# Kernel optimization log

Hardware: AMD Instinct MI355X
Metric: run time of the kernel (lower is better)

## Reference

```python
import jax, jax.numpy as jnp
import numpy as np

N = 100000   # nodes
E = 1000000  # edges per block
P = 100000   # pos/neg link edges
IN = 128
H = 64


def setup_inputs() -> dict:
    key = jax.random.key(0)
    ks = jax.random.split(key, 24)
    d = {}
    d["x"] = jax.random.normal(ks[0], (N, IN), jnp.float32)
    d["edge_weight"] = jax.random.uniform(ks[1], (3, E), jnp.float32)
    d["src"] = jax.random.randint(ks[2], (E,), 0, N)
    d["dst"] = jax.random.randint(ks[3], (E,), 0, N)
    d["pos_src"] = jax.random.randint(ks[4], (P,), 0, N)
    d["pos_dst"] = jax.random.randint(ks[5], (P,), 0, N)
    d["neg_src"] = jax.random.randint(ks[6], (P,), 0, N)
    d["neg_dst"] = jax.random.randint(ks[7], (P,), 0, N)
    s = 1.0 / np.sqrt(IN)
    h = 1.0 / np.sqrt(H)
    d["W0"] = jax.random.normal(ks[8], (IN, H), jnp.float32) * s
    d["b0"] = jnp.zeros((H,), jnp.float32)
    d["W1"] = jax.random.normal(ks[9], (H, H), jnp.float32) * h
    d["b1"] = jnp.zeros((H,), jnp.float32)
    d["W2"] = jax.random.normal(ks[10], (H, H), jnp.float32) * h
    d["b2"] = jnp.zeros((H,), jnp.float32)
    d["P0"] = jax.random.normal(ks[11], (H, H), jnp.float32) * h
    d["pb0"] = jnp.zeros((H,), jnp.float32)
    d["P1"] = jax.random.normal(ks[12], (H, H), jnp.float32) * h
    d["pb1"] = jnp.zeros((H,), jnp.float32)
    d["P2"] = jax.random.normal(ks[13], (H, 1), jnp.float32) * h
    d["pb2"] = jnp.zeros((1,), jnp.float32)
    return d


def _graph_conv(h, W, b, src, dst, ew, n_nodes):
    # DGL GraphConv, norm='both': D_out^{-1/2} on source feats,
    # edge-weighted sum aggregation, D_in^{-1/2} on result, then linear.
    ones = jnp.ones(src.shape[0], h.dtype)
    deg_out = jax.ops.segment_sum(ones, src, num_segments=n_nodes)
    deg_in = jax.ops.segment_sum(ones, dst, num_segments=n_nodes)
    norm_src = jax.lax.rsqrt(jnp.maximum(deg_out, 1.0))
    norm_dst = jax.lax.rsqrt(jnp.maximum(deg_in, 1.0))
    # apply weight before aggregation (in_feats >= out_feats); math-equivalent either way
    hw = (h * norm_src[:, None]) @ W            # [N, H]
    msg = hw[src] * ew[:, None]                 # [E, H] gather + scale
    agg = jax.ops.segment_sum(msg, dst, num_segments=n_nodes)  # scatter-add
    return agg * norm_dst[:, None] + b


def reference(x, edge_weight, src, dst, pos_src, pos_dst, neg_src, neg_dst,
              W0, b0, W1, b1, W2, b2, P0, pb0, P1, pb1, P2, pb2):
    h = jax.nn.relu(_graph_conv(x, W0, b0, src, dst, edge_weight[0], N))
    h = jax.nn.relu(_graph_conv(h, W1, b1, src, dst, edge_weight[1], N))
    h = _graph_conv(h, W2, b2, src, dst, edge_weight[2], N)  # no relu on last layer

    def mlp(z):
        z = jax.nn.relu(z @ P0 + pb0)
        z = jax.nn.relu(z @ P1 + pb1)
        return z @ P2 + pb2

    h_pos = mlp(h[pos_src] * h[pos_dst])  # [P, 1]
    h_neg = mlp(h[neg_src] * h[neg_dst])  # [P, 1]
    return (h_pos, h_neg)
```

## Files before the change

### kernel.cpp

```cpp
#include <hip/hip_runtime.h>


#define NN 100000
#define NE 1000000
#define NP 100000
#define SCAN_NB 98

__device__ __forceinline__ void row_fma(float4& acc, float xv, const float4& wv) {
    acc.x = fmaf(xv, wv.x, acc.x);
    acc.y = fmaf(xv, wv.y, acc.y);
    acc.z = fmaf(xv, wv.z, acc.z);
    acc.w = fmaf(xv, wv.w, acc.w);
}

__global__ void deg_kernel(const int4* __restrict__ src4, const int4* __restrict__ dst4,
                           int* __restrict__ repl, int E4) {
    int xcc;
    asm volatile("s_getreg_b32 %0, hwreg(HW_REG_XCC_ID)" : "=s"(xcc));
    xcc &= 7;
    int* dout = repl + xcc * NN;
    int* din  = repl + (8 + xcc) * NN;
    int tid = blockIdx.x * blockDim.x + threadIdx.x;
    if (tid < E4) {
        int4 s = src4[tid], d = dst4[tid];
        __hip_atomic_fetch_add(&dout[s.x], 1, __ATOMIC_RELAXED, __HIP_MEMORY_SCOPE_WORKGROUP);
        __hip_atomic_fetch_add(&dout[s.y], 1, __ATOMIC_RELAXED, __HIP_MEMORY_SCOPE_WORKGROUP);
        __hip_atomic_fetch_add(&dout[s.z], 1, __ATOMIC_RELAXED, __HIP_MEMORY_SCOPE_WORKGROUP);
        __hip_atomic_fetch_add(&dout[s.w], 1, __ATOMIC_RELAXED, __HIP_MEMORY_SCOPE_WORKGROUP);
        __hip_atomic_fetch_add(&din[d.x], 1, __ATOMIC_RELAXED, __HIP_MEMORY_SCOPE_WORKGROUP);
        __hip_atomic_fetch_add(&din[d.y], 1, __ATOMIC_RELAXED, __HIP_MEMORY_SCOPE_WORKGROUP);
        __hip_atomic_fetch_add(&din[d.z], 1, __ATOMIC_RELAXED, __HIP_MEMORY_SCOPE_WORKGROUP);
        __hip_atomic_fetch_add(&din[d.w], 1, __ATOMIC_RELAXED, __HIP_MEMORY_SCOPE_WORKGROUP);
    }
}

__global__ void reduce_norm_kernel(const int* __restrict__ repl, float* __restrict__ norm_src,
                                   float* __restrict__ norm_dst, int* __restrict__ deg_in, int n) {
    int i = blockIdx.x * blockDim.x + threadIdx.x;
    if (i < n) {
        int so = 0, si = 0;
#pragma unroll
        for (int x = 0; x < 8; ++x) {
            so += repl[x * NN + i];
            si += repl[(8 + x) * NN + i];
        }
        norm_src[i] = rsqrtf(fmaxf((float)so, 1.0f));
        norm_dst[i] = rsqrtf(fmaxf((float)si, 1.0f));
        deg_in[i] = si;
    }
}

__global__ __launch_bounds__(1024) void scan_block(const int* __restrict__ deg,
                                                   int* __restrict__ tmp_excl,
                                                   int* __restrict__ blocksums, int n) {
    __shared__ int wsums[16];
    const int i = blockIdx.x * 1024 + threadIdx.x;
    const int lane = threadIdx.x & 63, w = threadIdx.x >> 6;
    int v = (i < n) ? deg[i] : 0;
    int s = v;
#pragma unroll
    for (int off = 1; off < 64; off <<= 1) {
        int u = __shfl_up(s, off, 64);
        if (lane >= off) s += u;
    }
    if (lane == 63) wsums[w] = s;
    __syncthreads();
    if (w == 0) {
        int wv = (lane < 16) ? wsums[lane] : 0;
#pragma unroll
        for (int off = 1; off < 16; off <<= 1) {
            int u = __shfl_up(wv, off, 64);
            if (lane >= off) wv += u;
        }
        if (lane < 16) wsums[lane] = wv;
    }
    __syncthreads();
    int excl = s - v + (w > 0 ? wsums[w - 1] : 0);
    if (i < n) tmp_excl[i] = excl;
    if (threadIdx.x == 1023) blocksums[blockIdx.x] = excl + v;
}

__global__ void scan_sums(int* __restrict__ bs, int nb) {
    __shared__ int wtot[2];
    const int t = threadIdx.x;
    const int lane = t & 63, w = t >> 6;
    int v = (t < nb) ? bs[t] : 0;
    int s = v;
#pragma unroll
    for (int off = 1; off < 64; off <<= 1) {
        int u = __shfl_up(s, off, 64);
        if (lane >= off) s += u;
    }
    if (lane == 63) wtot[w] = s;
    __syncthreads();
    int excl = s - v + (w == 1 ? wtot[0] : 0);
    if (t < nb) bs[t] = excl;
}

__global__ __launch_bounds__(1024) void scan_apply(const int* __restrict__ tmp_excl,
                                                   const int* __restrict__ bs,
                                                   int* __restrict__ row_ptr,
                                                   int* __restrict__ cursor, int n) {
    const int i = blockIdx.x * 1024 + threadIdx.x;
    if (i < n) {
        int r = tmp_excl[i] + bs[blockIdx.x];
        row_ptr[i] = r;
        cursor[i] = r;
    }
    if (i == 0) row_ptr[n] = NE;
}

__global__ void csr_fill(const int* __restrict__ src, const int* __restrict__ dst,
                         const float* __restrict__ ew, const float* __restrict__ norm_src,
                         int* __restrict__ cursor, float4* __restrict__ cedge, int E) {
    int tid = blockIdx.x * blockDim.x + threadIdx.x;
    int stride = gridDim.x * blockDim.x;
    for (int e = tid; e < E; e += stride) {
        int s = src[e];
        int d = dst[e];
        float nsv = norm_src[s];
        int slot = atomicAdd(&cursor[d], 1);
        float4 c;
        c.x = __int_as_float(s);
        c.y = ew[e] * nsv;
        c.z = ew[NE + e] * nsv;
        c.w = ew[2 * NE + e] * nsv;
        cedge[slot] = c;
    }
}

template <int WSEL, bool RELU>
__global__ __launch_bounds__(256) void aggregate(const float* __restrict__ hw,
                                                 const float4* __restrict__ cedge,
                                                 const int* __restrict__ row_ptr,
                                                 const float* __restrict__ norm_dst,
                                                 const float* __restrict__ bias,
                                                 float* __restrict__ outx, int n) {
    const int lane = threadIdx.x & 63;
    const int gw = (blockIdx.x * blockDim.x + threadIdx.x) >> 6;
    const int nw = (gridDim.x * blockDim.x) >> 6;
    const float blane = bias[lane];
    for (int node = gw; node < n; node += nw) {
        int beg = row_ptr[node], end = row_ptr[node + 1];
        float a0 = 0.f, a1 = 0.f, a2 = 0.f, a3 = 0.f;
        int i = beg;
        for (; i + 7 < end; i += 8) {
            float4 c0 = cedge[i + 0], c1 = cedge[i + 1], c2 = cedge[i + 2], c3 = cedge[i + 3];
            float4 c4 = cedge[i + 4], c5 = cedge[i + 5], c6 = cedge[i + 6], c7 = cedge[i + 7];
            float h0 = hw[__float_as_int(c0.x) * 64 + lane];
            float h1 = hw[__float_as_int(c1.x) * 64 + lane];
            float h2 = hw[__float_as_int(c2.x) * 64 + lane];
            float h3 = hw[__float_as_int(c3.x) * 64 + lane];
            float h4 = hw[__float_as_int(c4.x) * 64 + lane];
            float h5 = hw[__float_as_int(c5.x) * 64 + lane];
            float h6 = hw[__float_as_int(c6.x) * 64 + lane];
            float h7 = hw[__float_as_int(c7.x) * 64 + lane];
            a0 = fmaf(h0, (WSEL == 0) ? c0.y : (WSEL == 1) ? c0.z : c0.w, a0);
            a1 = fmaf(h1, (WSEL == 0) ? c1.y : (WSEL == 1) ? c1.z : c1.w, a1);
            a2 = fmaf(h2, (WSEL == 0) ? c2.y : (WSEL == 1) ? c2.z : c2.w, a2);
            a3 = fmaf(h3, (WSEL == 0) ? c3.y : (WSEL == 1) ? c3.z : c3.w, a3);
            a0 = fmaf(h4, (WSEL == 0) ? c4.y : (WSEL == 1) ? c4.z : c4.w, a0);
            a1 = fmaf(h5, (WSEL == 0) ? c5.y : (WSEL == 1) ? c5.z : c5.w, a1);
            a2 = fmaf(h6, (WSEL == 0) ? c6.y : (WSEL == 1) ? c6.z : c6.w, a2);
            a3 = fmaf(h7, (WSEL == 0) ? c7.y : (WSEL == 1) ? c7.z : c7.w, a3);
        }
        for (; i + 1 < end; i += 2) {
            float4 c0 = cedge[i], c1 = cedge[i + 1];
            float h0 = hw[__float_as_int(c0.x) * 64 + lane];
            float h1 = hw[__float_as_int(c1.x) * 64 + lane];
            a0 = fmaf(h0, (WSEL == 0) ? c0.y : (WSEL == 1) ? c0.z : c0.w, a0);
            a1 = fmaf(h1, (WSEL == 0) ? c1.y : (WSEL == 1) ? c1.z : c1.w, a1);
        }
        if (i < end) {
            float4 c0 = cedge[i];
            float h0 = hw[__float_as_int(c0.x) * 64 + lane];
            a0 = fmaf(h0, (WSEL == 0) ? c0.y : (WSEL == 1) ? c0.z : c0.w, a0);
        }
        float a = (a0 + a1) + (a2 + a3);
        float t = fmaf(a, norm_dst[node], blane);
        if (RELU) t = fmaxf(t, 0.f);
        outx[node * 64 + lane] = t;
    }
}

template <int K>
__global__ __launch_bounds__(256, 5) void gemm_tile(const float* __restrict__ in,
                                                    const float* __restrict__ W,
                                                    float* __restrict__ out, int n) {
    __shared__ float Ws[K * 64];
    const int tid = threadIdx.x;
    for (int i = tid; i < K * 16; i += 256) ((float4*)Ws)[i] = ((const float4*)W)[i];
    __syncthreads();

    const int tr = tid >> 4, tc = tid & 15;
    const int row0 = blockIdx.x * 64 + tr * 4;
    const float* xr0 = in + (size_t)min(row0 + 0, n - 1) * K;
    const float* xr1 = in + (size_t)min(row0 + 1, n - 1) * K;
    const float* xr2 = in + (size_t)min(row0 + 2, n - 1) * K;
    const float* xr3 = in + (size_t)min(row0 + 3, n - 1) * K;

    float4 acc0 = {0, 0, 0, 0}, acc1 = {0, 0, 0, 0}, acc2 = {0, 0, 0, 0}, acc3 = {0, 0, 0, 0};
#pragma unroll 4
    for (int k4 = 0; k4 < K / 4; ++k4) {
        const int kb = k4 * 4;
        float4 xv0 = *(const float4*)&xr0[kb];
        float4 xv1 = *(const float4*)&xr1[kb];
        float4 xv2 = *(const float4*)&xr2[kb];
        float4 xv3 = *(const float4*)&xr3[kb];
        const float* wb = &Ws[kb * 64 + tc * 4];
        float4 wk;
        wk = *(const float4*)(wb);
        row_fma(acc0, xv0.x, wk); row_fma(acc1, xv1.x, wk); row_fma(acc2, xv2.x, wk); row_fma(acc3, xv3.x, wk);
        wk = *(const float4*)(wb + 64);
        row_fma(acc0, xv0.y, wk); row_fma(acc1, xv1.y, wk); row_fma(acc2, xv2.y, wk); row_fma(acc3, xv3.y, wk);
        wk = *(const float4*)(wb + 128);
        row_fma(acc0, xv0.z, wk); row_fma(acc1, xv1.z, wk); row_fma(acc2, xv2.z, wk); row_fma(acc3, xv3.z, wk);
        wk = *(const float4*)(wb + 192);
        row_fma(acc0, xv0.w, wk); row_fma(acc1, xv1.w, wk); row_fma(acc2, xv2.w, wk); row_fma(acc3, xv3.w, wk);
    }

#pragma unroll
    for (int i = 0; i < 4; ++i) {
        int row = row0 + i;
        if (row < n) {
            float4 o = (i == 0) ? acc0 : (i == 1) ? acc1 : (i == 2) ? acc2 : acc3;
            *(float4*)&out[row * 64 + tc * 4] = o;
        }
    }
}

#define ZST 76

__global__ __launch_bounds__(256) void mlp_tile(const float* __restrict__ hfin,
                                                const float* __restrict__ P0,
                                                const float* __restrict__ pb0,
                                                const float* __restrict__ P1,
                                                const float* __restrict__ pb1,
                                                const float* __restrict__ P2,
                                                const float* __restrict__ pb2,
                                                const int* __restrict__ pos_src,
                                                const int* __restrict__ pos_dst,
                                                const int* __restrict__ neg_src,
                                                const int* __restrict__ neg_dst,
                                                float* __restrict__ out, int P) {
    __shared__ float Zs[64][ZST];
    __shared__ float pb0s[64], pb1s[64], P2s[64];
    __shared__ int pas[64], pbs[64];
    const int tid = threadIdx.x;
    const int base = blockIdx.x << 6;
    if (tid < 64) {
        pb0s[tid] = pb0[tid];
        pb1s[tid] = pb1[tid];
        P2s[tid] = P2[tid];
        int p = base + tid;
        pas[tid] = (p < P) ? pos_src[p] : neg_src[p - P];
        pbs[tid] = (p < P) ? pos_dst[p] : neg_dst[p - P];
    }
    const float pb2v = pb2[0];
    const int lane = tid & 63, w = tid >> 6;
    const int tr = tid >> 4, tc = tid & 15;
    __syncthreads();

    {
        const int sub = lane >> 4;
        const int c4 = (lane & 15) * 4;
        float4 ha[4], hb[4];
#pragma unroll
        for (int r = 0; r < 4; ++r) {
            const int pi = w * 16 + r * 4 + sub;
            ha[r] = *(const float4*)&hfin[pas[pi] * 64 + c4];
            hb[r] = *(const float4*)&hfin[pbs[pi] * 64 + c4];
        }
#pragma unroll
        for (int r = 0; r < 4; ++r) {
            const int pi = w * 16 + r * 4 + sub;
            float4 z;
            z.x = ha[r].x * hb[r].x;
            z.y = ha[r].y * hb[r].y;
            z.z = ha[r].z * hb[r].z;
            z.w = ha[r].w * hb[r].w;
            *(float4*)&Zs[pi][c4] = z;
        }
    }
    __syncthreads();

    float4 acc0, acc1, acc2, acc3;
    {
        float4 binit = *(const float4*)&pb0s[tc * 4];
        acc0 = binit; acc1 = binit; acc2 = binit; acc3 = binit;
    }
#pragma unroll 4
    for (int k4 = 0; k4 < 16; ++k4) {
        const int kb = k4 * 4;
        float4 xv0 = *(const float4*)&Zs[tr * 4 + 0][kb];
        float4 xv1 = *(const float4*)&Zs[tr * 4 + 1][kb];
        float4 xv2 = *(const float4*)&Zs[tr * 4 + 2][kb];
        float4 xv3 = *(const float4*)&Zs[tr * 4 + 3][kb];
        const float* wb = &P0[kb * 64 + tc * 4];
        float4 wk;
        wk = *(const float4*)(wb);
        row_fma(acc0, xv0.x, wk); row_fma(acc1, xv1.x, wk); row_fma(acc2, xv2.x, wk); row_fma(acc3, xv3.x, wk);
        wk = *(const float4*)(wb + 64);
        row_fma(acc0, xv0.y, wk); row_fma(acc1, xv1.y, wk); row_fma(acc2, xv2.y, wk); row_fma(acc3, xv3.y, wk);
        wk = *(const float4*)(wb + 128);
        row_fma(acc0, xv0.z, wk); row_fma(acc1, xv1.z, wk); row_fma(acc2, xv2.z, wk); row_fma(acc3, xv3.z, wk);
        wk = *(const float4*)(wb + 192);
        row_fma(acc0, xv0.w, wk); row_fma(acc1, xv1.w, wk); row_fma(acc2, xv2.w, wk); row_fma(acc3, xv3.w, wk);
    }
    __syncthreads();
#pragma unroll
    for (int i = 0; i < 4; ++i) {
        float4 o = (i == 0) ? acc0 : (i == 1) ? acc1 : (i == 2) ? acc2 : acc3;
        o.x = fmaxf(o.x, 0.f); o.y = fmaxf(o.y, 0.f); o.z = fmaxf(o.z, 0.f); o.w = fmaxf(o.w, 0.f);
        *(float4*)&Zs[tr * 4 + i][tc * 4] = o;
    }
    __syncthreads();

    {
        float4 binit = *(const float4*)&pb1s[tc * 4];
        acc0 = binit; acc1 = binit; acc2 = binit; acc3 = binit;
    }
#pragma unroll 4
    for (int k4 = 0; k4 < 16; ++k4) {
        const int kb = k4 * 4;
        float4 xv0 = *(const float4*)&Zs[tr * 4 + 0][kb];
        float4 xv1 = *(const float4*)&Zs[tr * 4 + 1][kb];
        float4 xv2 = *(const float4*)&Zs[tr * 4 + 2][kb];
        float4 xv3 = *(const float4*)&Zs[tr * 4 + 3][kb];
        const float* wb = &P1[kb * 64 + tc * 4];
        float4 wk;
        wk = *(const float4*)(wb);
        row_fma(acc0, xv0.x, wk); row_fma(acc1, xv1.x, wk); row_fma(acc2, xv2.x, wk); row_fma(acc3, xv3.x, wk);
        wk = *(const float4*)(wb + 64);
        row_fma(acc0, xv0.y, wk); row_fma(acc1, xv1.y, wk); row_fma(acc2, xv2.y, wk); row_fma(acc3, xv3.y, wk);
        wk = *(const float4*)(wb + 128);
        row_fma(acc0, xv0.z, wk); row_fma(acc1, xv1.z, wk); row_fma(acc2, xv2.z, wk); row_fma(acc3, xv3.z, wk);
        wk = *(const float4*)(wb + 192);
        row_fma(acc0, xv0.w, wk); row_fma(acc1, xv1.w, wk); row_fma(acc2, xv2.w, wk); row_fma(acc3, xv3.w, wk);
    }
    __syncthreads();
#pragma unroll
    for (int i = 0; i < 4; ++i) {
        float4 o = (i == 0) ? acc0 : (i == 1) ? acc1 : (i == 2) ? acc2 : acc3;
        o.x = fmaxf(o.x, 0.f); o.y = fmaxf(o.y, 0.f); o.z = fmaxf(o.z, 0.f); o.w = fmaxf(o.w, 0.f);
        *(float4*)&Zs[tr * 4 + i][tc * 4] = o;
    }
    __syncthreads();

    {
        int p = tid >> 2, kq = tid & 3;
        float s = 0.f;
#pragma unroll
        for (int i = 0; i < 16; ++i) s = fmaf(Zs[p][kq * 16 + i], P2s[kq * 16 + i], s);
        s += __shfl_xor(s, 1, 64);
        s += __shfl_xor(s, 2, 64);
        if (kq == 0) out[base + p] = s + pb2v;
    }
}

extern "C" void kernel_launch(void* const* d_in, const int* in_sizes, int n_in,
                              void* d_out, int out_size, void* d_ws, size_t ws_size,
                              hipStream_t stream) {
    const float* x     = (const float*)d_in[0];
    const float* ew    = (const float*)d_in[1];
    const int* src     = (const int*)d_in[2];
    const int* dst     = (const int*)d_in[3];
    const int* pos_src = (const int*)d_in[4];
    const int* pos_dst = (const int*)d_in[5];
    const int* neg_src = (const int*)d_in[6];
    const int* neg_dst = (const int*)d_in[7];
    const float* W0    = (const float*)d_in[8];
    const float* b0    = (const float*)d_in[9];
    const float* W1    = (const float*)d_in[10];
    const float* b1    = (const float*)d_in[11];
    const float* W2    = (const float*)d_in[12];
    const float* b2    = (const float*)d_in[13];
    const float* P0    = (const float*)d_in[14];
    const float* pb0   = (const float*)d_in[15];
    const float* P1    = (const float*)d_in[16];
    const float* pb1   = (const float*)d_in[17];
    const float* P2    = (const float*)d_in[18];
    const float* pb2   = (const float*)d_in[19];
    float* out = (float*)d_out;

    float* ws = (float*)d_ws;
    float* norm_src = ws;
    float* norm_dst = ws + 100000;
    int* cursor     = (int*)(ws + 200000);
    int* deg_in     = (int*)(ws + 300000);
    int* row_ptr    = (int*)(ws + 400000);
    float4* cedge   = (float4*)(ws + 500004);
    float* hw       = ws + 4500004;
    float* agg      = ws + 10900004;

    int* repl      = (int*)hw;
    int* tmp_excl  = (int*)hw + 16 * NN;
    int* blocksums = (int*)hw + 17 * NN;

    hipMemsetAsync(repl, 0, 16 * NN * sizeof(int), stream);
    deg_kernel<<<(NE / 4 + 255) / 256, 256, 0, stream>>>((const int4*)src, (const int4*)dst,
                                                         repl, NE / 4);
    reduce_norm_kernel<<<(NN + 255) / 256, 256, 0, stream>>>(repl, norm_src, norm_dst, deg_in, NN);
    scan_block<<<SCAN_NB, 1024, 0, stream>>>(deg_in, tmp_excl, blocksums, NN);
    scan_sums<<<1, 128, 0, stream>>>(blocksums, SCAN_NB);
    scan_apply<<<SCAN_NB, 1024, 0, stream>>>(tmp_excl, blocksums, row_ptr, cursor, NN);
    csr_fill<<<2048, 256, 0, stream>>>(src, dst, ew, norm_src, cursor, cedge, NE);

    const int NT = (NN + 63) / 64;

    gemm_tile<128><<<NT, 256, 0, stream>>>(x, W0, hw, NN);
    aggregate<0, true><<<4096, 256, 0, stream>>>(hw, cedge, row_ptr, norm_dst, b0, agg, NN);
    gemm_tile<64><<<NT, 256, 0, stream>>>(agg, W1, hw, NN);
    aggregate<1, true><<<4096, 256, 0, stream>>>(hw, cedge, row_ptr, norm_dst, b1, agg, NN);
    gemm_tile<64><<<NT, 256, 0, stream>>>(agg, W2, hw, NN);
    aggregate<2, false><<<4096, 256, 0, stream>>>(hw, cedge, row_ptr, norm_dst, b2, agg, NN);

    mlp_tile<<<(2 * NP) / 64, 256, 0, stream>>>(agg, P0, pb0, P1, pb1, P2, pb2,
                                                pos_src, pos_dst, neg_src, neg_dst, out, NP);
}
```

Before: 475.8 us.

## Fuse CSR fill and first-layer GEMM into one launch with split block roles

Merges the CSR edge-fill scatter and the layer-0 node GEMM (x @ W0) into one kernel. The first NT blocks do the GEMM tiles and the remaining blocks do the grid-strided atomic CSR fill, so the two independent phases can run concurrently. This is meant to overlap the compute-bound GEMM with the latency-bound atomic scatter and to remove one launch boundary. In exchange, every block reserves 32KB of shared memory for the W tile, including the CSR blocks that never use it, which may limit how many CSR blocks fit per CU.

After: 450.1 us. 5.4% less time.

```diff
diff --git a/kernel.cpp b/kernel.cpp
--- a/kernel.cpp
+++ b/kernel.cpp
@@ -5,6 +5,8 @@
 #define NE 1000000
 #define NP 100000
 #define SCAN_NB 98
+#define NT 1563
+#define CSRB 2048
 
 __device__ __forceinline__ void row_fma(float4& acc, float xv, const float4& wv) {
     acc.x = fmaf(xv, wv.x, acc.x);
@@ -110,22 +112,69 @@
     if (i == 0) row_ptr[n] = NE;
 }
 
-__global__ void csr_fill(const int* __restrict__ src, const int* __restrict__ dst,
-                         const float* __restrict__ ew, const float* __restrict__ norm_src,
-                         int* __restrict__ cursor, float4* __restrict__ cedge, int E) {
-    int tid = blockIdx.x * blockDim.x + threadIdx.x;
-    int stride = gridDim.x * blockDim.x;
-    for (int e = tid; e < E; e += stride) {
-        int s = src[e];
-        int d = dst[e];
-        float nsv = norm_src[s];
-        int slot = atomicAdd(&cursor[d], 1);
-        float4 c;
-        c.x = __int_as_float(s);
-        c.y = ew[e] * nsv;
-        c.z = ew[NE + e] * nsv;
-        c.w = ew[2 * NE + e] * nsv;
-        cedge[slot] = c;
+__global__ __launch_bounds__(256) void csr_gemm0_fused(
+        const int* __restrict__ src, const int* __restrict__ dst,
+        const float* __restrict__ ew, const float* __restrict__ norm_src,
+        int* __restrict__ cursor, float4* __restrict__ cedge,
+        const float* __restrict__ in, const float* __restrict__ W,
+        float* __restrict__ out, int n) {
+    __shared__ float Ws[128 * 64];
+    const int tid = threadIdx.x;
+
+    if (blockIdx.x < NT) {
+        for (int i = tid; i < 128 * 16; i += 256) ((float4*)Ws)[i] = ((const float4*)W)[i];
+        __syncthreads();
+
+        const int tr = tid >> 4, tc = tid & 15;
+        const int row0 = blockIdx.x * 64 + tr * 4;
+        const float* xr0 = in + (size_t)min(row0 + 0, n - 1) * 128;
+        const float* xr1 = in + (size_t)min(row0 + 1, n - 1) * 128;
+        const float* xr2 = in + (size_t)min(row0 + 2, n - 1) * 128;
+        const float* xr3 = in + (size_t)min(row0 + 3, n - 1) * 128;
+
+        float4 acc0 = {0, 0, 0, 0}, acc1 = {0, 0, 0, 0}, acc2 = {0, 0, 0, 0}, acc3 = {0, 0, 0, 0};
+#pragma unroll 4
+        for (int k4 = 0; k4 < 32; ++k4) {
+            const int kb = k4 * 4;
+            float4 xv0 = *(const float4*)&xr0[kb];
+            float4 xv1 = *(const float4*)&xr1[kb];
+            float4 xv2 = *(const float4*)&xr2[kb];
+            float4 xv3 = *(const float4*)&xr3[kb];
+            const float* wb = &Ws[kb * 64 + tc * 4];
+            float4 wk;
+            wk = *(const float4*)(wb);
+            row_fma(acc0, xv0.x, wk); row_fma(acc1, xv1.x, wk); row_fma(acc2, xv2.x, wk); row_fma(acc3, xv3.x, wk);
+            wk = *(const float4*)(wb + 64);
+            row_fma(acc0, xv0.y, wk); row_fma(acc1, xv1.y, wk); row_fma(acc2, xv2.y, wk); row_fma(acc3, xv3.y, wk);
+            wk = *(const float4*)(wb + 128);
+            row_fma(acc0, xv0.z, wk); row_fma(acc1, xv1.z, wk); row_fma(acc2, xv2.z, wk); row_fma(acc3, xv3.z, wk);
+            wk = *(const float4*)(wb + 192);
+            row_fma(acc0, xv0.w, wk); row_fma(acc1, xv1.w, wk); row_fma(acc2, xv2.w, wk); row_fma(acc3, xv3.w, wk);
+        }
+
+#pragma unroll
+        for (int i = 0; i < 4; ++i) {
+            int row = row0 + i;
+            if (row < n) {
+                float4 o = (i == 0) ? acc0 : (i == 1) ? acc1 : (i == 2) ? acc2 : acc3;
+                *(float4*)&out[row * 64 + tc * 4] = o;
+            }
+        }
+    } else {
+        int t = (blockIdx.x - NT) * 256 + tid;
+        int stride = CSRB * 256;
+        for (int e = t; e < NE; e += stride) {
+            int s = src[e];
+            int d = dst[e];
+            float nsv = norm_src[s];
+            int slot = atomicAdd(&cursor[d], 1);
+            float4 c;
+            c.x = __int_as_float(s);
+            c.y = ew[e] * nsv;
+            c.z = ew[NE + e] * nsv;
+            c.w = ew[2 * NE + e] * nsv;
+            cedge[slot] = c;
+        }
     }
 }
 
@@ -404,11 +453,10 @@
     scan_block<<<SCAN_NB, 1024, 0, stream>>>(deg_in, tmp_excl, blocksums, NN);
     scan_sums<<<1, 128, 0, stream>>>(blocksums, SCAN_NB);
     scan_apply<<<SCAN_NB, 1024, 0, stream>>>(tmp_excl, blocksums, row_ptr, cursor, NN);
-    csr_fill<<<2048, 256, 0, stream>>>(src, dst, ew, norm_src, cursor, cedge, NE);
-
-    const int NT = (NN + 63) / 64;
-
-    gemm_tile<128><<<NT, 256, 0, stream>>>(x, W0, hw, NN);
+
+    csr_gemm0_fused<<<NT + CSRB, 256, 0, stream>>>(src, dst, ew, norm_src, cursor, cedge,
+                                                   x, W0, hw, NN);
+
     aggregate<0, true><<<4096, 256, 0, stream>>>(hw, cedge, row_ptr, norm_dst, b0, agg, NN);
     gemm_tile<64><<<NT, 256, 0, stream>>>(agg, W1, hw, NN);
     aggregate<1, true><<<4096, 256, 0, stream>>>(hw, cedge, row_ptr, norm_dst, b1, agg, NN);
```
